# Performance work log

Hardware: AMD Instinct MI355X
Metric: run time of the kernel (lower is better)

## Reference

```python
import jax, jax.numpy as jnp
import numpy as np

N, Z_DIM = 131072, 64
K_CODES = 2048
QUANT_TEMP = 0.0  # default T when 'quant_temp' not passed


def setup_inputs() -> dict:
    key = jax.random.key(0)
    k1, k2 = jax.random.split(key)
    z = jax.random.normal(k1, (N, Z_DIM), dtype=jnp.float32)
    e = jax.random.normal(k2, (K_CODES, Z_DIM), dtype=jnp.float32)
    return {"z": z, "e": e}


def reference(z, e):
    # torch.cdist -> euclidean distance matrix [N, K]; argmin over squared
    # distance gives identical indices (sqrt is monotone), so skip the sqrt.
    # ||z - e||^2 = ||z||^2 - 2 z.e^T + ||e||^2
    z_sq = jnp.sum(z * z, axis=1, keepdims=True)          # [N, 1]
    e_sq = jnp.sum(e * e, axis=1)                          # [K]
    d2 = z_sq - 2.0 * (z @ e.T) + e_sq[None, :]            # [N, K]
    min_indices = jnp.argmin(d2, axis=1)                   # [N] int
    z_q = e[min_indices]                                   # gather [N, Z]
    commit_loss = jnp.mean((z - z_q) ** 2)                 # F.mse_loss
    # straight-through: z + (1 - T) * stop_grad(z_q - z), T = 0
    z_out = z + (1.0 - QUANT_TEMP) * jax.lax.stop_gradient(z_q - z)
    return z_out, min_indices, commit_loss
```

## Files before the change

kernel.cpp:

```cpp
#include <hip/hip_runtime.h>


#define N_ROWS 131072
#define ZD 64
#define KCODES 2048
#define RF 4
#define EPS_S 2e-3f
#define FLAG_CAP 32768

using bf16x8  = __attribute__((ext_vector_type(8))) short;
using floatx4 = __attribute__((ext_vector_type(4))) float;

__device__ inline float bf2f(unsigned short u) {
    union { unsigned int i; float f; } c; c.i = ((unsigned int)u) << 16; return c.f;
}
__device__ inline unsigned short f2bf(float x) {
    union { float f; unsigned int i; } c; c.f = x;
    unsigned int b = c.i + 0x7FFFu + ((c.i >> 16) & 1u);
    return (unsigned short)(b >> 16);
}


__global__ void prep_kernel(const float* __restrict__ e, float* __restrict__ ws) {
    int t = threadIdx.x, lane = t & 63, w = t >> 6;
    if (blockIdx.x == 0 && t == 0) { ws[0] = 0.0f; ((unsigned int*)ws)[1] = 0u; }
    int c = blockIdx.x * 4 + w;
    float* esn = ws + 1024;
    double* esq64 = (double*)((char*)ws + 16384);
    unsigned short* et = (unsigned short*)((char*)ws + 32768);
    float* eT = (float*)((char*)ws + 557056);

    float x = e[(size_t)c * ZD + lane];
    unsigned short h = f2bf(x);
    unsigned short l = f2bf(x - bf2f(h));
    size_t base = ((size_t)(c >> 4) << 11) + ((lane >> 3) << 7) + ((c & 15) << 3) + (lane & 7);
    et[base]        = h;
    et[base + 1024] = l;
    eT[lane * KCODES + c] = x;
    double s = (double)x * (double)x;
    for (int off = 1; off < 64; off <<= 1) s += __shfl_xor(s, off, 64);
    if (lane == 0) { esq64[c] = s; esn[c] = (float)(-0.5 * s); }
}

#define COMPUTE(H0, H1, L0, L1, EN, TT) do {                                 \
    float _fcol = (float)((TT) * 16 + lrow);                                 \
    floatx4 _ai = {EN, EN, EN, EN};                                          \
    floatx4 _zi = {0.0f, 0.0f, 0.0f, 0.0f};                                  \
    _Pragma("unroll")                                                        \
    for (int _rf = 0; _rf < RF; _rf++) {                                     \
        floatx4 acc  = _ai;                                                  \
        floatx4 acc2 = _zi;                                                  \
        acc  = __builtin_amdgcn_mfma_f32_16x16x32_bf16(Ah[_rf][0], H0, acc,  0, 0, 0); \
        acc2 = __builtin_amdgcn_mfma_f32_16x16x32_bf16(Ah[_rf][1], H1, acc2, 0, 0, 0); \
        acc  = __builtin_amdgcn_mfma_f32_16x16x32_bf16(Ah[_rf][0], L0, acc,  0, 0, 0); \
        acc2 = __builtin_amdgcn_mfma_f32_16x16x32_bf16(Ah[_rf][1], L1, acc2, 0, 0, 0); \
        acc  = __builtin_amdgcn_mfma_f32_16x16x32_bf16(Al[_rf][0], H0, acc,  0, 0, 0); \
        acc2 = __builtin_amdgcn_mfma_f32_16x16x32_bf16(Al[_rf][1], H1, acc2, 0, 0, 0); \
        _Pragma("unroll")                                                    \
        for (int _r = 0; _r < 4; _r++) {                                     \
            float _s  = acc[_r] + acc2[_r];                                  \
            bool  _gt = _s > mval[_rf][_r];                                  \
            mv2[_rf][_r]  = __builtin_amdgcn_fmed3f(_s, mval[_rf][_r], mv2[_rf][_r]); \
            midx[_rf][_r] = _gt ? _fcol : midx[_rf][_r];                     \
            mval[_rf][_r] = fmaxf(_s, mval[_rf][_r]);                        \
        }                                                                    \
    }                                                                        \
} while (0)

#define STAGE(BUF, TILE) do {                                                \
    const char* _src = (const char*)etiles + ((size_t)(TILE) << 12)          \
                       + ((size_t)threadIdx.x << 4);                         \
    __builtin_amdgcn_global_load_lds(                                        \
        (const __attribute__((address_space(1))) unsigned int*)_src,         \
        (__attribute__((address_space(3))) unsigned int*)&tilebuf[BUF][w << 10], \
        16, 0, 0);                                                           \
} while (0)

#define ITER(BUF, CT) do {                                                   \
    int _nt = ((CT) + 1) & 127;                                              \
    STAGE((BUF) ^ 1, _nt);                                                   \
    float _nen = esn[_nt * 16 + lrow];                                       \
    bf16x8 h0 = *(const bf16x8*)(const void*)(tilebuf[BUF] + (lane << 4));   \
    bf16x8 h1 = *(const bf16x8*)(const void*)(tilebuf[BUF] + 1024 + (lane << 4)); \
    bf16x8 l0 = *(const bf16x8*)(const void*)(tilebuf[BUF] + 2048 + (lane << 4)); \
    bf16x8 l1 = *(const bf16x8*)(const void*)(tilebuf[BUF] + 3072 + (lane << 4)); \
    COMPUTE(h0, h1, l0, l1, cen, CT);                                        \
    __syncthreads();                                                         \
    cen = _nen;                                                              \
} while (0)

__global__ __launch_bounds__(256, 2) void vq_mfma(
        const float* __restrict__ z, const float* __restrict__ e,
        float* __restrict__ ws, float* __restrict__ out) {
    const float* esn = ws + 1024;
    const char* etiles = (const char*)ws + 32768;
    unsigned int* cntp  = (unsigned int*)ws + 1;
    unsigned int* flags = (unsigned int*)((char*)ws + 1081344);

    __shared__ __attribute__((aligned(16))) char tilebuf[2][4096];

    int lane = threadIdx.x & 63;
    int w    = threadIdx.x >> 6;
    int wid  = blockIdx.x * 4 + w;
    int row0 = wid * (RF * 16);
    int lrow = lane & 15;
    int lq   = lane >> 4;

    bf16x8 Ah[RF][2], Al[RF][2];
#pragma unroll
    for (int rf = 0; rf < RF; rf++)
#pragma unroll
        for (int kc = 0; kc < 2; kc++) {
            const float* zp = z + (size_t)(row0 + rf * 16 + lrow) * ZD + kc * 32 + lq * 8;
            float xv[8];
            *(float4*)(void*)&xv[0] = *(const float4*)(const void*)zp;
            *(float4*)(void*)&xv[4] = *(const float4*)(const void*)(zp + 4);
            bf16x8 h, l;
#pragma unroll
            for (int j = 0; j < 8; j++) {
                unsigned short hb = f2bf(xv[j]);
                h[j] = (short)hb;
                l[j] = (short)f2bf(xv[j] - bf2f(hb));
            }
            Ah[rf][kc] = h; Al[rf][kc] = l;
            asm volatile("" : "+v"(Ah[rf][kc]), "+v"(Al[rf][kc]));
        }

    floatx4 mval[RF], mv2[RF], midx[RF];
#pragma unroll
    for (int rf = 0; rf < RF; rf++)
#pragma unroll
        for (int r = 0; r < 4; r++) {
            mval[rf][r] = -3.0e38f; mv2[rf][r] = -3.0e38f; midx[rf][r] = 0.0f;
        }

    STAGE(0, 0);
    float cen = esn[lrow];
    __syncthreads();

    for (int ct = 0; ct < 128; ct += 2) {
        ITER(0, ct);
        ITER(1, ct + 1);
    }

    float lacc = 0.0f;
#pragma unroll
    for (int rf = 0; rf < RF; rf++)
#pragma unroll
        for (int r = 0; r < 4; r++) {
            float v = mval[rf][r], v2 = mv2[rf][r], fi = midx[rf][r];
            for (int off = 1; off < 16; off <<= 1) {
                float ov  = __shfl_xor(v,  off, 64);
                float ofi = __shfl_xor(fi, off, 64);
                float ov2 = __shfl_xor(v2, off, 64);
                bool take = (ov > v) || ((ov == v) && (ofi < fi));
                float loser = take ? v : ov;
                v2 = fmaxf(fmaxf(v2, ov2), loser);
                v  = take ? ov  : v;
                fi = take ? ofi : fi;
            }
            int row = row0 + rf * 16 + lq * 4 + r;
            int idx = (int)fi;
            float4 ev = ((const float4*)(const void*)(e + (size_t)idx * ZD))[lrow];
            float4 zv = ((const float4*)(const void*)(z + (size_t)row * ZD))[lrow];
            ((float4*)(void*)(out + (size_t)row * ZD))[lrow] = ev;
            float dx = ev.x - zv.x, dy = ev.y - zv.y;
            float dz = ev.z - zv.z, dw = ev.w - zv.w;
            lacc = fmaf(dx, dx, lacc); lacc = fmaf(dy, dy, lacc);
            lacc = fmaf(dz, dz, lacc); lacc = fmaf(dw, dw, lacc);
            if (lrow == 0) {
                out[(size_t)N_ROWS * ZD + row] = fi;
                if (v - v2 < EPS_S) {
                    unsigned int i = atomicAdd(cntp, 1u);
                    if (i < FLAG_CAP) flags[i] = (unsigned int)row;
                }
            }
        }

    for (int off = 1; off < 64; off <<= 1) lacc += __shfl_xor(lacc, off, 64);
    __shared__ float sm[4];
    if (lane == 0) sm[w] = lacc;
    __syncthreads();
    if (threadIdx.x == 0) atomicAdd(ws, sm[0] + sm[1] + sm[2] + sm[3]);
}

__global__ __launch_bounds__(256) void vq_fixup(
        const float* __restrict__ z, const float* __restrict__ e,
        float* __restrict__ ws, float* __restrict__ out) {
    const double* esq64 = (const double*)((const char*)ws + 16384);
    const float* eT = (const float*)((const char*)ws + 557056);
    const unsigned int* flags = (const unsigned int*)((const char*)ws + 1081344);
    unsigned int cnt = ((const unsigned int*)ws)[1];
    if (cnt > FLAG_CAP) cnt = FLAG_CAP;

    __shared__ float zrow[ZD];
    __shared__ double sd[4]; __shared__ int si[4]; __shared__ int sbest;
    int t = threadIdx.x, lane = t & 63, w = t >> 6;

    for (unsigned int u = blockIdx.x; u < cnt; u += gridDim.x) {
        int row = (int)flags[u];
        __syncthreads();
        if (t < ZD) zrow[t] = z[(size_t)row * ZD + t];
        __syncthreads();

        double dacc[8];
#pragma unroll
        for (int j = 0; j < 8; j++) dacc[j] = 0.0;
        for (int k = 0; k < ZD; k++) {
            double zk = (double)zrow[k];
            const float* ek = eT + k * KCODES + t;
#pragma unroll
            for (int j = 0; j < 8; j++)
                dacc[j] = fma(zk, (double)ek[256 * j], dacc[j]);
        }
        double dmin = 1.0e300; int imin = 0;
#pragma unroll
        for (int j = 0; j < 8; j++) {
            int c = t + 256 * j;
            double d = fma(-2.0, dacc[j], esq64[c]);
            if (d < dmin) { dmin = d; imin = c; }
        }
        for (int off = 1; off < 64; off <<= 1) {
            double od = __shfl_xor(dmin, off, 64);
            int    oi = __shfl_xor(imin, off, 64);
            if (od < dmin || (od == dmin && oi < imin)) { dmin = od; imin = oi; }
        }
        if (lane == 0) { sd[w] = dmin; si[w] = imin; }
        __syncthreads();
        if (t == 0) {
            double bd = sd[0]; int bi = si[0];
            for (int q = 1; q < 4; q++)
                if (sd[q] < bd || (sd[q] == bd && si[q] < bi)) { bd = sd[q]; bi = si[q]; }
            sbest = bi;
        }
        __syncthreads();
        int bi = sbest;
        if (t < 16)
            ((float4*)(void*)(out + (size_t)row * ZD))[t] =
                ((const float4*)(const void*)(e + (size_t)bi * ZD))[t];
        if (t == 0) out[(size_t)N_ROWS * ZD + row] = (float)bi;
    }
}

__global__ void finalize_kernel(const float* __restrict__ ws,
                                float* __restrict__ out) {
    out[(size_t)N_ROWS * ZD + N_ROWS] = ws[0] * (1.0f / 8388608.0f);
}

extern "C" void kernel_launch(void* const* d_in, const int* in_sizes, int n_in,
                              void* d_out, int out_size, void* d_ws, size_t ws_size,
                              hipStream_t stream) {
    const float* z = (const float*)d_in[0];
    const float* e = (const float*)d_in[1];
    float* out = (float*)d_out;
    float* ws  = (float*)d_ws;

    prep_kernel<<<dim3(512), dim3(256), 0, stream>>>(e, ws);
    vq_mfma<<<dim3(512), dim3(256), 0, stream>>>(z, e, ws, out);
    vq_fixup<<<dim3(256), dim3(256), 0, stream>>>(z, e, ws, out);
    finalize_kernel<<<dim3(1), dim3(1), 0, stream>>>(ws, out);
}
```

Before: 198.2 us.

## Stage two codebook tiles per barrier, cache norms in LDS, drop finalize kernel

The main loop now stages two 16-code tiles per buffer, so each __syncthreads covers two compute steps instead of one, halving barrier count. The negated code norms are copied into LDS once per block rather than read from global memory every iteration. The column index is carried as an incrementing float, and the scalar loss write moves into the fixup kernel, removing one launch. LDS use per block doubles for the tile buffers and adds 8 KB for the norms. Writing the loss in fixup relies on the atomic sum being complete once the previous kernel on the stream finishes.

New measurement: 196.6 us. No clear change (-0.8%).

```diff
diff --git a/kernel.cpp b/kernel.cpp
--- a/kernel.cpp
+++ b/kernel.cpp
@@ -42,8 +42,7 @@
     if (lane == 0) { esq64[c] = s; esn[c] = (float)(-0.5 * s); }
 }
 
-#define COMPUTE(H0, H1, L0, L1, EN, TT) do {                                 \
-    float _fcol = (float)((TT) * 16 + lrow);                                 \
+#define COMPUTE(H0, H1, L0, L1, EN, FCOL) do {                               \
     floatx4 _ai = {EN, EN, EN, EN};                                          \
     floatx4 _zi = {0.0f, 0.0f, 0.0f, 0.0f};                                  \
     _Pragma("unroll")                                                        \
@@ -61,43 +60,43 @@
             float _s  = acc[_r] + acc2[_r];                                  \
             bool  _gt = _s > mval[_rf][_r];                                  \
             mv2[_rf][_r]  = __builtin_amdgcn_fmed3f(_s, mval[_rf][_r], mv2[_rf][_r]); \
-            midx[_rf][_r] = _gt ? _fcol : midx[_rf][_r];                     \
+            midx[_rf][_r] = _gt ? (FCOL) : midx[_rf][_r];                    \
             mval[_rf][_r] = fmaxf(_s, mval[_rf][_r]);                        \
         }                                                                    \
     }                                                                        \
 } while (0)
 
-#define STAGE(BUF, TILE) do {                                                \
-    const char* _src = (const char*)etiles + ((size_t)(TILE) << 12)          \
-                       + ((size_t)threadIdx.x << 4);                         \
+#define STAGE2(BUF, TILE) do {                                               \
+    const char* _s0 = etiles + ((size_t)((TILE) & 127) << 12)                \
+                      + ((size_t)threadIdx.x << 4);                          \
+    const char* _s1 = etiles + ((size_t)(((TILE) + 1) & 127) << 12)          \
+                      + ((size_t)threadIdx.x << 4);                          \
     __builtin_amdgcn_global_load_lds(                                        \
-        (const __attribute__((address_space(1))) unsigned int*)_src,         \
+        (const __attribute__((address_space(1))) unsigned int*)_s0,          \
         (__attribute__((address_space(3))) unsigned int*)&tilebuf[BUF][w << 10], \
         16, 0, 0);                                                           \
+    __builtin_amdgcn_global_load_lds(                                        \
+        (const __attribute__((address_space(1))) unsigned int*)_s1,          \
+        (__attribute__((address_space(3))) unsigned int*)&tilebuf[BUF][4096 + (w << 10)], \
+        16, 0, 0);                                                           \
 } while (0)
 
-#define ITER(BUF, CT) do {                                                   \
-    int _nt = ((CT) + 1) & 127;                                              \
-    STAGE((BUF) ^ 1, _nt);                                                   \
-    float _nen = esn[_nt * 16 + lrow];                                       \
-    bf16x8 h0 = *(const bf16x8*)(const void*)(tilebuf[BUF] + (lane << 4));   \
-    bf16x8 h1 = *(const bf16x8*)(const void*)(tilebuf[BUF] + 1024 + (lane << 4)); \
-    bf16x8 l0 = *(const bf16x8*)(const void*)(tilebuf[BUF] + 2048 + (lane << 4)); \
-    bf16x8 l1 = *(const bf16x8*)(const void*)(tilebuf[BUF] + 3072 + (lane << 4)); \
-    COMPUTE(h0, h1, l0, l1, cen, CT);                                        \
-    __syncthreads();                                                         \
-    cen = _nen;                                                              \
+#define READT(BUF, OFS, H0, H1, L0, L1) do {                                 \
+    H0 = *(const bf16x8*)(const void*)(tilebuf[BUF] + (OFS) + (lane << 4));          \
+    H1 = *(const bf16x8*)(const void*)(tilebuf[BUF] + (OFS) + 1024 + (lane << 4));   \
+    L0 = *(const bf16x8*)(const void*)(tilebuf[BUF] + (OFS) + 2048 + (lane << 4));   \
+    L1 = *(const bf16x8*)(const void*)(tilebuf[BUF] + (OFS) + 3072 + (lane << 4));   \
 } while (0)
 
 __global__ __launch_bounds__(256, 2) void vq_mfma(
         const float* __restrict__ z, const float* __restrict__ e,
         float* __restrict__ ws, float* __restrict__ out) {
-    const float* esn = ws + 1024;
     const char* etiles = (const char*)ws + 32768;
     unsigned int* cntp  = (unsigned int*)ws + 1;
     unsigned int* flags = (unsigned int*)((char*)ws + 1081344);
 
-    __shared__ __attribute__((aligned(16))) char tilebuf[2][4096];
+    __shared__ __attribute__((aligned(16))) char tilebuf[2][8192];
+    __shared__ __attribute__((aligned(16))) float esn_sm[KCODES];
 
     int lane = threadIdx.x & 63;
     int w    = threadIdx.x >> 6;
@@ -105,6 +104,19 @@
     int row0 = wid * (RF * 16);
     int lrow = lane & 15;
     int lq   = lane >> 4;
+
+    {
+        const char* esrc = (const char*)ws + 4096 + ((size_t)threadIdx.x << 4);
+        __builtin_amdgcn_global_load_lds(
+            (const __attribute__((address_space(1))) unsigned int*)esrc,
+            (__attribute__((address_space(3))) unsigned int*)((char*)esn_sm + (w << 10)),
+            16, 0, 0);
+        __builtin_amdgcn_global_load_lds(
+            (const __attribute__((address_space(1))) unsigned int*)(esrc + 4096),
+            (__attribute__((address_space(3))) unsigned int*)((char*)esn_sm + 4096 + (w << 10)),
+            16, 0, 0);
+    }
+    STAGE2(0, 0);
 
     bf16x8 Ah[RF][2], Al[RF][2];
 #pragma unroll
@@ -134,13 +146,36 @@
             mval[rf][r] = -3.0e38f; mv2[rf][r] = -3.0e38f; midx[rf][r] = 0.0f;
         }
 
-    STAGE(0, 0);
-    float cen = esn[lrow];
+    float fcol = (float)lrow;
     __syncthreads();
 
-    for (int ct = 0; ct < 128; ct += 2) {
-        ITER(0, ct);
-        ITER(1, ct + 1);
+    for (int ct = 0; ct < 128; ct += 4) {
+        STAGE2(1, ct + 2);
+        {
+            float en0 = esn_sm[ct * 16 + lrow];
+            float en1 = esn_sm[ct * 16 + 16 + lrow];
+            bf16x8 h0, h1, l0, l1;
+            READT(0, 0, h0, h1, l0, l1);
+            COMPUTE(h0, h1, l0, l1, en0, fcol);
+            fcol += 16.0f;
+            READT(0, 4096, h0, h1, l0, l1);
+            COMPUTE(h0, h1, l0, l1, en1, fcol);
+            fcol += 16.0f;
+        }
+        __syncthreads();
+        STAGE2(0, ct + 4);
+        {
+            float en0 = esn_sm[ct * 16 + 32 + lrow];
+            float en1 = esn_sm[ct * 16 + 48 + lrow];
+            bf16x8 h0, h1, l0, l1;
+            READT(1, 0, h0, h1, l0, l1);
+            COMPUTE(h0, h1, l0, l1, en0, fcol);
+            fcol += 16.0f;
+            READT(1, 4096, h0, h1, l0, l1);
+            COMPUTE(h0, h1, l0, l1, en1, fcol);
+            fcol += 16.0f;
+        }
+        __syncthreads();
     }
 
     float lacc = 0.0f;
@@ -193,6 +228,9 @@
     unsigned int cnt = ((const unsigned int*)ws)[1];
     if (cnt > FLAG_CAP) cnt = FLAG_CAP;
 
+    if (blockIdx.x == 0 && threadIdx.x == 0)
+        out[(size_t)N_ROWS * ZD + N_ROWS] = ws[0] * (1.0f / 8388608.0f);
+
     __shared__ float zrow[ZD];
     __shared__ double sd[4]; __shared__ int si[4]; __shared__ int sbest;
     int t = threadIdx.x, lane = t & 63, w = t >> 6;
@@ -240,11 +278,6 @@
                 ((const float4*)(const void*)(e + (size_t)bi * ZD))[t];
         if (t == 0) out[(size_t)N_ROWS * ZD + row] = (float)bi;
     }
-}
-
-__global__ void finalize_kernel(const float* __restrict__ ws,
-                                float* __restrict__ out) {
-    out[(size_t)N_ROWS * ZD + N_ROWS] = ws[0] * (1.0f / 8388608.0f);
 }
 
 extern "C" void kernel_launch(void* const* d_in, const int* in_sizes, int n_in,
@@ -258,5 +291,4 @@
     prep_kernel<<<dim3(512), dim3(256), 0, stream>>>(e, ws);
     vq_mfma<<<dim3(512), dim3(256), 0, stream>>>(z, e, ws, out);
     vq_fixup<<<dim3(256), dim3(256), 0, stream>>>(z, e, ws, out);
-    finalize_kernel<<<dim3(1), dim3(1), 0, stream>>>(ws, out);
-}
+}
```

## Halve rows per wave, raise occupancy, preload codebook norms into LDS, drop finalize

Applied to the files above, without the earlier changes.

Each wave now handles 32 rows instead of 64, the grid doubles and launch bounds ask for 4 blocks per CU, so more waves are resident to hide latency. The negated codebook norms are copied once into shared memory with global_load_lds, so the inner loop no longer does a global load per tile. The column index is kept as a running float counter. The finalize kernel is folded into the fixup kernel, saving one launch. In exchange, each e tile staged into LDS is reused across fewer rows, so staging traffic per row doubles.

New measurement: 210.1 us. 1.06x slower.

```diff
diff --git a/kernel.cpp b/kernel.cpp
--- a/kernel.cpp
+++ b/kernel.cpp
@@ -4,7 +4,7 @@
 #define N_ROWS 131072
 #define ZD 64
 #define KCODES 2048
-#define RF 4
+#define RF 2
 #define EPS_S 2e-3f
 #define FLAG_CAP 32768
 
@@ -42,8 +42,7 @@
     if (lane == 0) { esq64[c] = s; esn[c] = (float)(-0.5 * s); }
 }
 
-#define COMPUTE(H0, H1, L0, L1, EN, TT) do {                                 \
-    float _fcol = (float)((TT) * 16 + lrow);                                 \
+#define COMPUTE(H0, H1, L0, L1, EN, FCOL) do {                               \
     floatx4 _ai = {EN, EN, EN, EN};                                          \
     floatx4 _zi = {0.0f, 0.0f, 0.0f, 0.0f};                                  \
     _Pragma("unroll")                                                        \
@@ -61,14 +60,14 @@
             float _s  = acc[_r] + acc2[_r];                                  \
             bool  _gt = _s > mval[_rf][_r];                                  \
             mv2[_rf][_r]  = __builtin_amdgcn_fmed3f(_s, mval[_rf][_r], mv2[_rf][_r]); \
-            midx[_rf][_r] = _gt ? _fcol : midx[_rf][_r];                     \
-            mval[_rf][_r] = fmaxf(_s, mval[_rf][_r]);                        \
+            midx[_rf][_r] = _gt ? (FCOL) : midx[_rf][_r];                    \
+            mval[_rf][_r] = fmaxf(_s, mval[_rf][_r]);                       \
         }                                                                    \
     }                                                                        \
 } while (0)
 
 #define STAGE(BUF, TILE) do {                                                \
-    const char* _src = (const char*)etiles + ((size_t)(TILE) << 12)          \
+    const char* _src = etiles + ((size_t)((TILE) & 127) << 12)               \
                        + ((size_t)threadIdx.x << 4);                         \
     __builtin_amdgcn_global_load_lds(                                        \
         (const __attribute__((address_space(1))) unsigned int*)_src,         \
@@ -77,27 +76,26 @@
 } while (0)
 
 #define ITER(BUF, CT) do {                                                   \
-    int _nt = ((CT) + 1) & 127;                                              \
-    STAGE((BUF) ^ 1, _nt);                                                   \
-    float _nen = esn[_nt * 16 + lrow];                                       \
+    STAGE((BUF) ^ 1, (CT) + 1);                                              \
+    float _en = esn_sm[(CT) * 16 + lrow];                                    \
     bf16x8 h0 = *(const bf16x8*)(const void*)(tilebuf[BUF] + (lane << 4));   \
     bf16x8 h1 = *(const bf16x8*)(const void*)(tilebuf[BUF] + 1024 + (lane << 4)); \
     bf16x8 l0 = *(const bf16x8*)(const void*)(tilebuf[BUF] + 2048 + (lane << 4)); \
     bf16x8 l1 = *(const bf16x8*)(const void*)(tilebuf[BUF] + 3072 + (lane << 4)); \
-    COMPUTE(h0, h1, l0, l1, cen, CT);                                        \
+    COMPUTE(h0, h1, l0, l1, _en, fcol);                                      \
+    fcol += 16.0f;                                                           \
     __syncthreads();                                                         \
-    cen = _nen;                                                              \
 } while (0)
 
-__global__ __launch_bounds__(256, 2) void vq_mfma(
+__global__ __launch_bounds__(256, 4) void vq_mfma(
         const float* __restrict__ z, const float* __restrict__ e,
         float* __restrict__ ws, float* __restrict__ out) {
-    const float* esn = ws + 1024;
     const char* etiles = (const char*)ws + 32768;
     unsigned int* cntp  = (unsigned int*)ws + 1;
     unsigned int* flags = (unsigned int*)((char*)ws + 1081344);
 
     __shared__ __attribute__((aligned(16))) char tilebuf[2][4096];
+    __shared__ __attribute__((aligned(16))) float esn_sm[KCODES];
 
     int lane = threadIdx.x & 63;
     int w    = threadIdx.x >> 6;
@@ -105,6 +103,19 @@
     int row0 = wid * (RF * 16);
     int lrow = lane & 15;
     int lq   = lane >> 4;
+
+    {
+        const char* esrc = (const char*)ws + 4096 + ((size_t)threadIdx.x << 4);
+        __builtin_amdgcn_global_load_lds(
+            (const __attribute__((address_space(1))) unsigned int*)esrc,
+            (__attribute__((address_space(3))) unsigned int*)((char*)esn_sm + (w << 10)),
+            16, 0, 0);
+        __builtin_amdgcn_global_load_lds(
+            (const __attribute__((address_space(1))) unsigned int*)(esrc + 4096),
+            (__attribute__((address_space(3))) unsigned int*)((char*)esn_sm + 4096 + (w << 10)),
+            16, 0, 0);
+    }
+    STAGE(0, 0);
 
     bf16x8 Ah[RF][2], Al[RF][2];
 #pragma unroll
@@ -134,8 +145,7 @@
             mval[rf][r] = -3.0e38f; mv2[rf][r] = -3.0e38f; midx[rf][r] = 0.0f;
         }
 
-    STAGE(0, 0);
-    float cen = esn[lrow];
+    float fcol = (float)lrow;
     __syncthreads();
 
     for (int ct = 0; ct < 128; ct += 2) {
@@ -193,6 +203,9 @@
     unsigned int cnt = ((const unsigned int*)ws)[1];
     if (cnt > FLAG_CAP) cnt = FLAG_CAP;
 
+    if (blockIdx.x == 0 && threadIdx.x == 0)
+        out[(size_t)N_ROWS * ZD + N_ROWS] = ws[0] * (1.0f / 8388608.0f);
+
     __shared__ float zrow[ZD];
     __shared__ double sd[4]; __shared__ int si[4]; __shared__ int sbest;
     int t = threadIdx.x, lane = t & 63, w = t >> 6;
@@ -240,11 +253,6 @@
                 ((const float4*)(const void*)(e + (size_t)bi * ZD))[t];
         if (t == 0) out[(size_t)N_ROWS * ZD + row] = (float)bi;
     }
-}
-
-__global__ void finalize_kernel(const float* __restrict__ ws,
-                                float* __restrict__ out) {
-    out[(size_t)N_ROWS * ZD + N_ROWS] = ws[0] * (1.0f / 8388608.0f);
 }
 
 extern "C" void kernel_launch(void* const* d_in, const int* in_sizes, int n_in,
@@ -256,7 +264,6 @@
     float* ws  = (float*)d_ws;
 
     prep_kernel<<<dim3(512), dim3(256), 0, stream>>>(e, ws);
-    vq_mfma<<<dim3(512), dim3(256), 0, stream>>>(z, e, ws, out);
+    vq_mfma<<<dim3(1024), dim3(256), 0, stream>>>(z, e, ws, out);
     vq_fixup<<<dim3(256), dim3(256), 0, stream>>>(z, e, ws, out);
-    finalize_kernel<<<dim3(1), dim3(1), 0, stream>>>(ws, out);
-}
+}
```
